# Performance work log

Hardware: AMD Instinct MI355X
Metric: run time of the kernel (lower is better)

The kernel has to match this reference:

```python
import jax, jax.numpy as jnp
import numpy as np

DIM = 256
D_STATE = 32
EXPAND = 2
E = EXPAND * DIM            # d_inner = 512
DT_RANK = (DIM + 15) // 16  # 16 (mamba default ceil(d_model/16))
D_CONV = 4                  # mamba default causal conv width
B = 4
L = 1024


def layernorm(x, g, b, eps=1e-5):
    m = jnp.mean(x, axis=-1, keepdims=True)
    v = jnp.var(x, axis=-1, keepdims=True)
    return (x - m) / jnp.sqrt(v + eps) * g + b


def dwconv(x_bcl, w, b, pad):
    # x_bcl: [B,C,L], w: [C,1,K] depthwise
    y = jax.lax.conv_general_dilated(
        x_bcl, w, window_strides=(1,), padding=[pad],
        feature_group_count=x_bcl.shape[1],
        dimension_numbers=('NCW', 'OIW', 'NCW'))
    return y + b[None, :, None]


def selective_scan(u, dt, A, Bm, Cm, D):
    # u,dt: [B,L,E]; A: [E,N]; Bm,Cm: [B,L,N]; D: [E]
    dA = jnp.exp(dt[..., None] * A)                                # [B,L,E,N]
    dBu = dt[..., None] * Bm[:, :, None, :] * u[..., None]         # [B,L,E,N]

    def step(h, inp):
        dA_t, dBu_t = inp
        h = dA_t * h + dBu_t
        return h, h

    h0 = jnp.zeros((u.shape[0], E, D_STATE), u.dtype)
    _, hs = jax.lax.scan(step, h0, (dA.transpose(1, 0, 2, 3), dBu.transpose(1, 0, 2, 3)))
    y = jnp.einsum('lben,bln->ble', hs, Cm)                        # [B,L,E]
    return y + u * D


def mamba(x, in_proj_w, ssm_conv_w, ssm_conv_b, x_proj_w,
          dt_proj_w, dt_proj_b, A_log, Dp, out_proj_w):
    xz = x @ in_proj_w.T                     # [B,L,2E]
    xin, z = xz[..., :E], xz[..., E:]
    # causal depthwise conv (pad left D_CONV-1) + SiLU
    xc = dwconv(xin.transpose(0, 2, 1), ssm_conv_w, ssm_conv_b, (D_CONV - 1, 0))
    u = jax.nn.silu(xc).transpose(0, 2, 1)   # [B,L,E]
    dbl = u @ x_proj_w.T                      # [B,L,dt_rank+2N]
    dt_r = dbl[..., :DT_RANK]
    Bm = dbl[..., DT_RANK:DT_RANK + D_STATE]
    Cm = dbl[..., DT_RANK + D_STATE:]
    dt = jax.nn.softplus(dt_r @ dt_proj_w.T + dt_proj_b)  # [B,L,E]
    A = -jnp.exp(A_log)                                    # [E,N]
    y = selective_scan(u, dt, A, Bm, Cm, Dp)
    y = y * jax.nn.silu(z)
    return y @ out_proj_w.T


def setup_inputs() -> dict:
    key = jax.random.key(0)
    ks = jax.random.split(key, 12)
    f = lambda k, s, sc=0.02: jax.random.normal(k, s, jnp.float32) * sc
    dt_init = jnp.exp(jax.random.uniform(ks[10], (E,), jnp.float32,
                                         np.log(1e-3), np.log(1e-1)))
    dt_bias = dt_init + jnp.log(-jnp.expm1(-dt_init))  # inverse softplus
    A_log = jnp.log(jnp.tile(jnp.arange(1, D_STATE + 1, dtype=jnp.float32), (E, 1)))
    return {
        'x': jax.random.normal(ks[0], (B, L, DIM), jnp.float32),
        'norm1_g': jnp.ones((DIM,), jnp.float32), 'norm1_b': jnp.zeros((DIM,), jnp.float32),
        'conv_w': f(ks[1], (DIM, 1, 3), 0.1), 'conv_b': jnp.zeros((DIM,), jnp.float32),
        'in_proj_w': f(ks[2], (2 * E, DIM)),
        'ssm_conv_w': f(ks[3], (E, 1, D_CONV), 0.1), 'ssm_conv_b': jnp.zeros((E,), jnp.float32),
        'x_proj_w': f(ks[4], (DT_RANK + 2 * D_STATE, E)),
        'dt_proj_w': f(ks[5], (E, DT_RANK), 0.1), 'dt_proj_b': dt_bias,
        'A_log': A_log, 'Dp': jnp.ones((E,), jnp.float32),
        'out_proj_w': f(ks[6], (DIM, E)),
        'norm2_g': jnp.ones((DIM,), jnp.float32), 'norm2_b': jnp.zeros((DIM,), jnp.float32),
        'mlp_w1': f(ks[7], (4 * DIM, DIM)), 'mlp_b1': jnp.zeros((4 * DIM,), jnp.float32),
        'mlp_w2': f(ks[8], (DIM, 4 * DIM)), 'mlp_b2': jnp.zeros((DIM,), jnp.float32),
    }


def reference(x, norm1_g, norm1_b, conv_w, conv_b, in_proj_w, ssm_conv_w,
              ssm_conv_b, x_proj_w, dt_proj_w, dt_proj_b, A_log, Dp,
              out_proj_w, norm2_g, norm2_b, mlp_w1, mlp_b1, mlp_w2, mlp_b2):
    res = x
    h = layernorm(x, norm1_g, norm1_b)
    # local depthwise conv, kernel 3, same padding
    h_conv = dwconv(h.transpose(0, 2, 1), conv_w, conv_b, (1, 1)).transpose(0, 2, 1)
    h = mamba(h_conv + h, in_proj_w, ssm_conv_w, ssm_conv_b, x_proj_w,
              dt_proj_w, dt_proj_b, A_log, Dp, out_proj_w)
    h = res + h  # drop_path = identity (eval)
    m = layernorm(h, norm2_g, norm2_b)
    m = jax.nn.gelu(m @ mlp_w1.T + mlp_b1, approximate=False) @ mlp_w2.T + mlp_b2
    return h + m
```

## Files before the change

### kernel.cpp

```cpp
#include <hip/hip_runtime.h>
#include <hip/hip_bf16.h>
#include <math.h>

#define BATCH 4
#define LSEQ  1024
#define DIM   256
#define ESZ   512
#define NST   32
#define RNK   16
#define MROWS 4096
#define NCH   64
#define CHL   16

typedef __attribute__((ext_vector_type(8))) short bf16x8;
typedef __attribute__((ext_vector_type(4))) float f32x4;

__device__ __forceinline__ float silu_f(float v) { return v / (1.f + __expf(-v)); }
__device__ __forceinline__ float softplus_f(float v) {
    return (v > 20.f) ? v : log1pf(__expf(v));
}
__device__ __forceinline__ float bs2f(short s) {
    union { unsigned int u; float f; } v;
    v.u = ((unsigned int)(unsigned short)s) << 16;
    return v.f;
}
__device__ __forceinline__ short f2bs(float f) {
    __hip_bfloat16 h = __float2bfloat16(f);
    return *(short*)&h;
}

template <int N> __device__ __forceinline__ void waitvm() {
    if constexpr (N == 0) asm volatile("s_waitcnt vmcnt(0)" ::: "memory");
    else if constexpr (N == 4) asm volatile("s_waitcnt vmcnt(4)" ::: "memory");
    else if constexpr (N == 6) asm volatile("s_waitcnt vmcnt(6)" ::: "memory");
    else if constexpr (N == 9) asm volatile("s_waitcnt vmcnt(9)" ::: "memory");
    else static_assert(N == 0, "add literal");
}
__device__ __forceinline__ void fence_sched() {
    __builtin_amdgcn_sched_barrier(0);
    asm volatile("" ::: "memory");
}

__global__ __launch_bounds__(256) void prep_kernel(
    const float* __restrict__ ipw, const float* __restrict__ opw,
    const float* __restrict__ w1,  const float* __restrict__ w2,
    const float* __restrict__ xpw, __hip_bfloat16* __restrict__ dst,
    const float* __restrict__ x, const float* __restrict__ g,
    const float* __restrict__ b, const float* __restrict__ cw,
    const float* __restrict__ cb, __hip_bfloat16* __restrict__ hm)
{
    if (blockIdx.x < 936) {
        int i = blockIdx.x * 256 + threadIdx.x;
        if (i >= 239616) return;
        const float* s; int off;
        if      (i < 65536)  { s = ipw; off = i; }
        else if (i < 98304)  { s = opw; off = i - 65536; }
        else if (i < 163840) { s = w1;  off = i - 98304; }
        else if (i < 229376) { s = w2;  off = i - 163840; }
        else                 { s = xpw; off = i - 229376; }
        float4 v = ((const float4*)s)[off];
        union { __hip_bfloat16 h[4]; short4 s4; } u;
        u.h[0] = __float2bfloat16(v.x);
        u.h[1] = __float2bfloat16(v.y);
        u.h[2] = __float2bfloat16(v.z);
        u.h[3] = __float2bfloat16(v.w);
        ((short4*)dst)[i] = u.s4;
        return;
    }
    const int row = blockIdx.x - 936;
    const int l   = row & (LSEQ - 1);
    const int d   = threadIdx.x;
    const float gc = g[d], bc = b[d];

    float xc = x[row * DIM + d];
    float xl = (l > 0)        ? x[(row - 1) * DIM + d] : 0.f;
    float xr = (l < LSEQ - 1) ? x[(row + 1) * DIM + d] : 0.f;

    float a[6] = { xc, xc * xc, xl, xl * xl, xr, xr * xr };
    #pragma unroll
    for (int o = 32; o > 0; o >>= 1)
        #pragma unroll
        for (int j = 0; j < 6; ++j) a[j] += __shfl_down(a[j], o, 64);
    __shared__ float red[4][6];
    if ((d & 63) == 0)
        #pragma unroll
        for (int j = 0; j < 6; ++j) red[d >> 6][j] = a[j];
    __syncthreads();
    float t[6];
    #pragma unroll
    for (int j = 0; j < 6; ++j)
        t[j] = red[0][j] + red[1][j] + red[2][j] + red[3][j];

    auto ln = [&](float v, float s, float s2) {
        float m  = s * (1.f / DIM);
        float vr = s2 * (1.f / DIM) - m * m;
        return (v - m) * rsqrtf(vr + 1e-5f) * gc + bc;
    };
    float ln_c = ln(xc, t[0], t[1]);
    float acc  = cw[d * 3 + 1] * ln_c + cb[d] + ln_c;
    if (l > 0)        acc += cw[d * 3 + 0] * ln(xl, t[2], t[3]);
    if (l < LSEQ - 1) acc += cw[d * 3 + 2] * ln(xr, t[4], t[5]);
    hm[row * DIM + d] = __float2bfloat16(acc);
}

#define EPI_NONE      0
#define EPI_GELU      2
#define EPI_RES       3
#define EPI_BIAS_RES  4

template <int BM, int BN, int EPI, int OUT_BF16>
__global__ __launch_bounds__(256) void gemm_lds(
    const __hip_bfloat16* __restrict__ A, int lda,
    const __hip_bfloat16* __restrict__ W, int ldw,
    void* __restrict__ Cout, int ldc, int K,
    const float* __restrict__ bias,
    const float* __restrict__ res, int ldres)
{
    constexpr int BK  = 64;
    constexpr int WTN = BN / 4;
    constexpr int BNF = WTN / 16;
    constexpr int AMF = BM / 16;
    constexpr int AIT = (BM * 8) / 256;
    constexpr int WIT = (BN * 8) / 256;
    constexpr int NLD = AIT + WIT;

    __shared__ __hip_bfloat16 As[2][BM * BK];
    __shared__ __hip_bfloat16 Ws[2][BN * BK];

    const int tid  = threadIdx.x;
    const int lane = tid & 63;
    const int wave = tid >> 6;
    const int wn   = wave * WTN;
    const int m0   = blockIdx.x * BM;
    const int n0   = blockIdx.y * BN;
    const int q    = lane >> 4;
    const int lr   = lane & 15;
    const int sx   = (lr & 7) << 4;

    const __hip_bfloat16* Ab = A + (long)m0 * lda;
    const __hip_bfloat16* Wb = W + (long)n0 * ldw;

    f32x4 acc[AMF][BNF];
    #pragma unroll
    for (int i = 0; i < AMF; ++i)
        #pragma unroll
        for (int j = 0; j < BNF; ++j)
            acc[i][j] = (f32x4){0.f, 0.f, 0.f, 0.f};

    auto stage = [&](int s, int k0) {
        #pragma unroll
        for (int it = 0; it < AIT; ++it) {
            const int g   = it * 256 + tid;
            const int row = g >> 3;
            const int scc = (g & 7) ^ (row & 7);
            __builtin_amdgcn_global_load_lds(
                (const __attribute__((address_space(1))) void*)
                    (Ab + (long)row * lda + k0 + scc * 8),
                (__attribute__((address_space(3))) void*)
                    (&As[s][(it * 256 + wave * 64) * 8]),
                16, 0, 0);
        }
        #pragma unroll
        for (int it = 0; it < WIT; ++it) {
            const int g   = it * 256 + tid;
            const int row = g >> 3;
            const int scc = (g & 7) ^ (row & 7);
            __builtin_amdgcn_global_load_lds(
                (const __attribute__((address_space(1))) void*)
                    (Wb + (long)row * ldw + k0 + scc * 8),
                (__attribute__((address_space(3))) void*)
                    (&Ws[s][(it * 256 + wave * 64) * 8]),
                16, 0, 0);
        }
    };

    stage(0, 0);
    if (BK < K) stage(1, BK);

    int cur = 0;
    for (int k0 = 0; k0 < K; k0 += BK) {
        if (k0 + BK < K) waitvm<NLD>(); else waitvm<0>();
        __builtin_amdgcn_s_barrier();
        fence_sched();
        #pragma unroll
        for (int ks = 0; ks < 2; ++ks) {
            const int co = (ks * 64 + q * 16) ^ sx;
            bf16x8 af[AMF], bfr[BNF];
            #pragma unroll
            for (int i = 0; i < AMF; ++i)
                af[i] = *(const bf16x8*)(
                    (const char*)&As[cur][0] + (i * 16 + lr) * 128 + co);
            #pragma unroll
            for (int j = 0; j < BNF; ++j)
                bfr[j] = *(const bf16x8*)(
                    (const char*)&Ws[cur][0] + (wn + j * 16 + lr) * 128 + co);
            #pragma unroll
            for (int i = 0; i < AMF; ++i)
                #pragma unroll
                for (int j = 0; j < BNF; ++j)
                    acc[i][j] = __builtin_amdgcn_mfma_f32_16x16x32_bf16(
                        af[i], bfr[j], acc[i][j], 0, 0, 0);
        }
        fence_sched();
        __builtin_amdgcn_s_barrier();
        fence_sched();
        if (k0 + 2 * BK < K) stage(cur, k0 + 2 * BK);
        cur ^= 1;
    }

    #pragma unroll
    for (int i = 0; i < AMF; ++i) {
        #pragma unroll
        for (int j = 0; j < BNF; ++j) {
            const int col  = n0 + wn + j * 16 + lr;
            const int rowb = m0 + i * 16 + q * 4;
            #pragma unroll
            for (int r = 0; r < 4; ++r) {
                const int row = rowb + r;
                float v = acc[i][j][r];
                if (EPI == EPI_GELU) {
                    v += bias[col];
                    v = 0.5f * v * (1.f + erff(v * 0.70710678118654752f));
                } else if (EPI == EPI_RES) {
                    v += res[(long)row * ldres + col];
                } else if (EPI == EPI_BIAS_RES) {
                    v += bias[col] + res[(long)row * ldres + col];
                }
                if (OUT_BF16)
                    ((__hip_bfloat16*)Cout)[(long)row * ldc + col] = __float2bfloat16(v);
                else
                    ((float*)Cout)[(long)row * ldc + col] = v;
            }
        }
    }
}

__global__ __launch_bounds__(256) void outproj_ln_kernel(
    const __hip_bfloat16* __restrict__ A,
    const __hip_bfloat16* __restrict__ W,
    const float* __restrict__ xres,
    const float* __restrict__ g, const float* __restrict__ b,
    float* __restrict__ hres,
    __hip_bfloat16* __restrict__ h1)
{
    constexpr int BM = 16, BN = 256, BK = 64, K = 512;
    constexpr int NLD = 9;
    __shared__ __hip_bfloat16 As[2][BM * BK];
    __shared__ __hip_bfloat16 Ws[2][BN * BK];
    __shared__ float lnt[BM][BN + 4];
    __shared__ float lnm[BM], lni[BM];

    const int tid  = threadIdx.x;
    const int lane = tid & 63;
    const int wave = tid >> 6;
    const int wn   = wave * 64;
    const int m0   = blockIdx.x * BM;
    const int q    = lane >> 4;
    const int lr   = lane & 15;
    const int sx   = (lr & 7) << 4;

    const __hip_bfloat16* Ab = A + (long)m0 * K;

    f32x4 acc[4];
    #pragma unroll
    for (int j = 0; j < 4; ++j) acc[j] = (f32x4){0.f, 0.f, 0.f, 0.f};

    auto stage = [&](int s, int k0) {
        {
            const int ch = wave * 32 + lane;
            if (lane < 32) {
                const int row = ch >> 3;
                const int scc = (ch & 7) ^ (row & 7);
                __builtin_amdgcn_global_load_lds(
                    (const __attribute__((address_space(1))) void*)
                        (Ab + (long)row * K + k0 + scc * 8),
                    (__attribute__((address_space(3))) void*)
                        (&As[s][(wave * 32) * 8]),
                    16, 0, 0);
            }
        }
        #pragma unroll
        for (int it = 0; it < 8; ++it) {
            const int gW  = it * 256 + tid;
            const int row = gW >> 3;
            const int scc = (gW & 7) ^ (row & 7);
            __builtin_amdgcn_global_load_lds(
                (const __attribute__((address_space(1))) void*)
                    (W + (long)row * K + k0 + scc * 8),
                (__attribute__((address_space(3))) void*)
                    (&Ws[s][(it * 256 + wave * 64) * 8]),
                16, 0, 0);
        }
    };

    stage(0, 0);
    stage(1, BK);

    int cur = 0;
    for (int k0 = 0; k0 < K; k0 += BK) {
        if (k0 + BK < K) waitvm<NLD>(); else waitvm<0>();
        __builtin_amdgcn_s_barrier();
        fence_sched();
        #pragma unroll
        for (int ks = 0; ks < 2; ++ks) {
            const int co = (ks * 64 + q * 16) ^ sx;
            bf16x8 af = *(const bf16x8*)((const char*)&As[cur][0] + lr * 128 + co);
            #pragma unroll
            for (int j = 0; j < 4; ++j) {
                bf16x8 bfr = *(const bf16x8*)(
                    (const char*)&Ws[cur][0] + (wn + j * 16 + lr) * 128 + co);
                acc[j] = __builtin_amdgcn_mfma_f32_16x16x32_bf16(af, bfr, acc[j], 0, 0, 0);
            }
        }
        fence_sched();
        __builtin_amdgcn_s_barrier();
        fence_sched();
        if (k0 + 2 * BK < K) stage(cur, k0 + 2 * BK);
        cur ^= 1;
    }

    #pragma unroll
    for (int j = 0; j < 4; ++j) {
        const int col = wn + j * 16 + lr;
        #pragma unroll
        for (int r = 0; r < 4; ++r) {
            const int row = q * 4 + r;
            float v = acc[j][r] + xres[(long)(m0 + row) * DIM + col];
            hres[(long)(m0 + row) * DIM + col] = v;
            lnt[row][col] = v;
        }
    }
    __syncthreads();

    {
        const int rr = tid >> 4, cc = tid & 15;
        float s = 0.f, s2 = 0.f;
        #pragma unroll
        for (int k = 0; k < 16; ++k) {
            float v = lnt[rr][cc + k * 16];
            s += v; s2 += v * v;
        }
        #pragma unroll
        for (int m = 8; m > 0; m >>= 1) {
            s  += __shfl_xor(s,  m, 64);
            s2 += __shfl_xor(s2, m, 64);
        }
        if (cc == 0) {
            float mean = s * (1.f / DIM);
            float var  = s2 * (1.f / DIM) - mean * mean;
            lnm[rr] = mean;
            lni[rr] = rsqrtf(var + 1e-5f);
        }
    }
    __syncthreads();

    #pragma unroll
    for (int j = 0; j < 4; ++j) {
        const int col = wn + j * 16 + lr;
        const float gc = g[col], bc = b[col];
        #pragma unroll
        for (int r = 0; r < 4; ++r) {
            const int row = q * 4 + r;
            float v = lnt[row][col];
            h1[(long)(m0 + row) * DIM + col] =
                __float2bfloat16((v - lnm[row]) * lni[row] * gc + bc);
        }
    }
}

__global__ __launch_bounds__(256) void xproj_conv_mfma(
    const __hip_bfloat16* __restrict__ xz,
    const float* __restrict__ scw, const float* __restrict__ scb,
    const __hip_bfloat16* __restrict__ W,
    float* __restrict__ C)
{
    constexpr int LS = 72;
    __shared__ __hip_bfloat16 As[64 * LS];
    __shared__ __hip_bfloat16 Ws[80 * LS];
    const int tid  = threadIdx.x;
    const int lane = tid & 63;
    const int wave = tid >> 6;
    const int wm   = wave * 16;
    const int m0   = blockIdx.x * 64;
    const int srow = tid >> 3;
    const int scol = (tid & 7) * 8;
    const int q    = lane >> 4;
    const int lr   = lane & 15;

    f32x4 acc[5];
    #pragma unroll
    for (int j = 0; j < 5; ++j) acc[j] = (f32x4){0.f, 0.f, 0.f, 0.f};

    auto mk_u2 = [&](int k0, bf16x8& u0, bf16x8& u1) {
        const int e0 = k0 + scol;
        float4 w4[8]; float cbv[8];
        #pragma unroll
        for (int j = 0; j < 8; ++j) {
            w4[j]  = *(const float4*)(scw + (e0 + j) * 4);
            cbv[j] = scb[e0 + j];
        }
        #pragma unroll
        for (int r = 0; r < 2; ++r) {
            const int bl = m0 + r * 32 + srow;
            const int l  = bl & (LSEQ - 1);
            const __hip_bfloat16* xp = xz + (long)bl * 1024 + e0;
            bf16x8 x3 = *(const bf16x8*)(xp);
            bf16x8 x0 = (l >= 3) ? *(const bf16x8*)(xp - 3 * 1024) : (bf16x8){0,0,0,0,0,0,0,0};
            bf16x8 x1 = (l >= 2) ? *(const bf16x8*)(xp - 2 * 1024) : (bf16x8){0,0,0,0,0,0,0,0};
            bf16x8 x2 = (l >= 1) ? *(const bf16x8*)(xp - 1 * 1024) : (bf16x8){0,0,0,0,0,0,0,0};
            bf16x8 o;
            #pragma unroll
            for (int j = 0; j < 8; ++j) {
                float a = cbv[j]
                    + w4[j].x * bs2f(x0[j]) + w4[j].y * bs2f(x1[j])
                    + w4[j].z * bs2f(x2[j]) + w4[j].w * bs2f(x3[j]);
                o[j] = f2bs(silu_f(a));
            }
            if (r == 0) u0 = o; else u1 = o;
        }
    };

    bf16x8 uc[2];
    float4 wr[3];
    mk_u2(0, uc[0], uc[1]);
    #pragma unroll
    for (int r = 0; r < 3; ++r) {
        int row = r * 32 + srow;
        wr[r] = (row < 80) ? *(const float4*)(W + (long)row * 512 + scol)
                           : make_float4(0.f, 0.f, 0.f, 0.f);
    }

    for (int k0 = 0; k0 < 512; k0 += 64) {
        __syncthreads();
        #pragma unroll
        for (int r = 0; r < 2; ++r)
            *(bf16x8*)(&As[(r * 32 + srow) * LS + scol]) = uc[r];
        #pragma unroll
        for (int r = 0; r < 3; ++r) {
            int row = r * 32 + srow;
            if (row < 80) *(float4*)(&Ws[row * LS + scol]) = wr[r];
        }
        __syncthreads();
        if (k0 + 64 < 512) {
            mk_u2(k0 + 64, uc[0], uc[1]);
            #pragma unroll
            for (int r = 0; r < 3; ++r) {
                int row = r * 32 + srow;
                if (row < 80)
                    wr[r] = *(const float4*)(W + (long)row * 512 + k0 + 64 + scol);
            }
        }
        #pragma unroll
        for (int ks = 0; ks < 2; ++ks) {
            bf16x8 af = *(const bf16x8*)(&As[(wm + lr) * LS + ks * 32 + q * 8]);
            #pragma unroll
            for (int j = 0; j < 5; ++j) {
                bf16x8 bf = *(const bf16x8*)(&Ws[(j * 16 + lr) * LS + ks * 32 + q * 8]);
                acc[j] = __builtin_amdgcn_mfma_f32_16x16x32_bf16(af, bf, acc[j], 0, 0, 0);
            }
        }
    }
    #pragma unroll
    for (int j = 0; j < 5; ++j)
        #pragma unroll
        for (int r = 0; r < 4; ++r)
            C[(long)(m0 + wm + q * 4 + r) * 80 + j * 16 + lr] = acc[j][r];
}

__global__ __launch_bounds__(256) void scan_s1(
    const __hip_bfloat16* __restrict__ xz, const float* __restrict__ dbl,
    const float* __restrict__ dtw, const float* __restrict__ dtb,
    const float* __restrict__ A_log,
    const float* __restrict__ scw, const float* __restrict__ scb,
    __hip_bfloat16* __restrict__ P, __hip_bfloat16* __restrict__ Q)
{
    const int tid = threadIdx.x;
    const int e  = ((blockIdx.x & 1) << 8) + tid;
    const int bc = blockIdx.x >> 1;
    const int c  = bc & (NCH - 1);
    const int b  = bc >> 6;

    __shared__ float sD[CHL][80];
    for (int g = tid; g < CHL * 20; g += 256) {
        int r = g / 20, cg = (g % 20) * 4;
        *(float4*)&sD[r][cg] =
            *(const float4*)(dbl + ((long)b * LSEQ + c * CHL + r) * 80 + cg);
    }

    float Aen[NST];
    #pragma unroll
    for (int qd = 0; qd < 8; ++qd) {
        float4 a4 = *(const float4*)(A_log + e * NST + qd * 4);
        Aen[qd * 4 + 0] = -__expf(a4.x);
        Aen[qd * 4 + 1] = -__expf(a4.y);
        Aen[qd * 4 + 2] = -__expf(a4.z);
        Aen[qd * 4 + 3] = -__expf(a4.w);
    }
    float cw4[4];
    #pragma unroll
    for (int k = 0; k < 4; ++k) cw4[k] = scw[e * 4 + k];
    const float cbe = scb[e];

    float4 wq[4];
    #pragma unroll
    for (int qd = 0; qd < 4; ++qd)
        wq[qd] = *(const float4*)(dtw + e * RNK + qd * 4);
    const float dtbe = dtb[e];

    const int l0 = c * CHL;
    const long rowbase = ((long)b * LSEQ) * 1024 + e;
    float xw0, xw1, xw2;
    if (c == 0) { xw0 = xw1 = xw2 = 0.f; }
    else {
        xw0 = __bfloat162float(xz[rowbase + (long)(l0 - 3) * 1024]);
        xw1 = __bfloat162float(xz[rowbase + (long)(l0 - 2) * 1024]);
        xw2 = __bfloat162float(xz[rowbase + (long)(l0 - 1) * 1024]);
    }

    float Pv[NST], Qv[NST];
    #pragma unroll
    for (int n = 0; n < NST; ++n) { Pv[n] = 1.f; Qv[n] = 0.f; }
    __syncthreads();

    for (int t = 0; t < CHL; ++t) {
        const int l = l0 + t;
        float xw3 = __bfloat162float(xz[rowbase + (long)l * 1024]);
        float u = silu_f(cbe + cw4[0]*xw0 + cw4[1]*xw1 + cw4[2]*xw2 + cw4[3]*xw3);
        xw0 = xw1; xw1 = xw2; xw2 = xw3;

        float4 d0 = *(const float4*)&sD[t][0];
        float4 d1 = *(const float4*)&sD[t][4];
        float4 d2 = *(const float4*)&sD[t][8];
        float4 d3 = *(const float4*)&sD[t][12];
        float raw = dtbe
            + wq[0].x*d0.x + wq[0].y*d0.y + wq[0].z*d0.z + wq[0].w*d0.w
            + wq[1].x*d1.x + wq[1].y*d1.y + wq[1].z*d1.z + wq[1].w*d1.w
            + wq[2].x*d2.x + wq[2].y*d2.y + wq[2].z*d2.z + wq[2].w*d2.w
            + wq[3].x*d3.x + wq[3].y*d3.y + wq[3].z*d3.z + wq[3].w*d3.w;
        float dt = softplus_f(raw);
        float xx = dt * u;

        #pragma unroll
        for (int qd = 0; qd < 8; ++qd) {
            float4 b4 = *(const float4*)&sD[t][16 + qd * 4];
            #pragma unroll
            for (int j = 0; j < 4; ++j) {
                const int n = qd * 4 + j;
                float bn = (j == 0) ? b4.x : (j == 1) ? b4.y : (j == 2) ? b4.z : b4.w;
                float dA = __expf(dt * Aen[n]);
                Pv[n] *= dA;
                Qv[n] = fmaf(dA, Qv[n], xx * bn);
            }
        }
    }
    const long pb = ((long)(b * NCH + c) * NST) * ESZ + e;
    #pragma unroll
    for (int n = 0; n < NST; ++n) {
        P[pb + (long)n * ESZ] = __float2bfloat16(Pv[n]);
        Q[pb + (long)n * ESZ] = __float2bfloat16(Qv[n]);
    }
}

__global__ __launch_bounds__(256) void scan_s2(
    __hip_bfloat16* __restrict__ P, const __hip_bfloat16* __restrict__ Q)
{
    const int tg = blockIdx.x * 256 + threadIdx.x;
    const int e  = tg & (ESZ - 1);
    const int n  = (tg >> 9) & (NST - 1);
    const int b  = tg >> 14;
    float h = 0.f;
    #pragma unroll 16
    for (int c = 0; c < NCH; ++c) {
        const long idx = ((long)(b * NCH + c) * NST + n) * ESZ + e;
        float Pv = __bfloat162float(P[idx]);
        float Qv = __bfloat162float(Q[idx]);
        P[idx] = __float2bfloat16(h);
        h = fmaf(Pv, h, Qv);
    }
}

__global__ __launch_bounds__(256) void scan_s3(
    const __hip_bfloat16* __restrict__ xz, const float* __restrict__ dbl,
    const float* __restrict__ dtw, const float* __restrict__ dtb,
    const float* __restrict__ A_log,
    const float* __restrict__ scw, const float* __restrict__ scb,
    const float* __restrict__ Dp, const __hip_bfloat16* __restrict__ H,
    __hip_bfloat16* __restrict__ yg)
{
    const int tid = threadIdx.x;
    const int e  = ((blockIdx.x & 1) << 8) + tid;
    const int bc = blockIdx.x >> 1;
    const int c  = bc & (NCH - 1);
    const int b  = bc >> 6;

    __shared__ float sD[CHL][80];
    for (int g = tid; g < CHL * 20; g += 256) {
        int r = g / 20, cg = (g % 20) * 4;
        *(float4*)&sD[r][cg] =
            *(const float4*)(dbl + ((long)b * LSEQ + c * CHL + r) * 80 + cg);
    }

    float Aen[NST];
    #pragma unroll
    for (int qd = 0; qd < 8; ++qd) {
        float4 a4 = *(const float4*)(A_log + e * NST + qd * 4);
        Aen[qd * 4 + 0] = -__expf(a4.x);
        Aen[qd * 4 + 1] = -__expf(a4.y);
        Aen[qd * 4 + 2] = -__expf(a4.z);
        Aen[qd * 4 + 3] = -__expf(a4.w);
    }
    float cw4[4];
    #pragma unroll
    for (int k = 0; k < 4; ++k) cw4[k] = scw[e * 4 + k];
    const float cbe = scb[e];
    const float dpe = Dp[e];

    float4 wq[4];
    #pragma unroll
    for (int qd = 0; qd < 4; ++qd)
        wq[qd] = *(const float4*)(dtw + e * RNK + qd * 4);
    const float dtbe = dtb[e];

    float h[NST];
    const long pb = ((long)(b * NCH + c) * NST) * ESZ + e;
    #pragma unroll
    for (int n = 0; n < NST; ++n)
        h[n] = __bfloat162float(H[pb + (long)n * ESZ]);

    const int l0 = c * CHL;
    const long rowbase = ((long)b * LSEQ) * 1024 + e;
    float xw0, xw1, xw2;
    if (c == 0) { xw0 = xw1 = xw2 = 0.f; }
    else {
        xw0 = __bfloat162float(xz[rowbase + (long)(l0 - 3) * 1024]);
        xw1 = __bfloat162float(xz[rowbase + (long)(l0 - 2) * 1024]);
        xw2 = __bfloat162float(xz[rowbase + (long)(l0 - 1) * 1024]);
    }
    __syncthreads();

    for (int t = 0; t < CHL; ++t) {
        const int l = l0 + t;
        const long bl = (long)b * LSEQ + l;
        float xw3 = __bfloat162float(xz[rowbase + (long)l * 1024]);
        float u = silu_f(cbe + cw4[0]*xw0 + cw4[1]*xw1 + cw4[2]*xw2 + cw4[3]*xw3);
        xw0 = xw1; xw1 = xw2; xw2 = xw3;

        float4 d0 = *(const float4*)&sD[t][0];
        float4 d1 = *(const float4*)&sD[t][4];
        float4 d2 = *(const float4*)&sD[t][8];
        float4 d3 = *(const float4*)&sD[t][12];
        float raw = dtbe
            + wq[0].x*d0.x + wq[0].y*d0.y + wq[0].z*d0.z + wq[0].w*d0.w
            + wq[1].x*d1.x + wq[1].y*d1.y + wq[1].z*d1.z + wq[1].w*d1.w
            + wq[2].x*d2.x + wq[2].y*d2.y + wq[2].z*d2.z + wq[2].w*d2.w
            + wq[3].x*d3.x + wq[3].y*d3.y + wq[3].z*d3.z + wq[3].w*d3.w;
        float dt = softplus_f(raw);
        float xx = dt * u;

        float y = 0.f;
        #pragma unroll
        for (int qd = 0; qd < 8; ++qd) {
            float4 b4 = *(const float4*)&sD[t][16 + qd * 4];
            float4 c4 = *(const float4*)&sD[t][48 + qd * 4];
            #pragma unroll
            for (int j = 0; j < 4; ++j) {
                const int n = qd * 4 + j;
                float bn = (j == 0) ? b4.x : (j == 1) ? b4.y : (j == 2) ? b4.z : b4.w;
                float cn = (j == 0) ? c4.x : (j == 1) ? c4.y : (j == 2) ? c4.z : c4.w;
                float dA = __expf(dt * Aen[n]);
                h[n] = fmaf(dA, h[n], xx * bn);
                y = fmaf(h[n], cn, y);
            }
        }
        y += u * dpe;
        float z = __bfloat162float(xz[rowbase + (long)l * 1024 + ESZ]);
        yg[bl * ESZ + e] = __float2bfloat16(y * silu_f(z));
    }
}

extern "C" void kernel_launch(void* const* d_in, const int* in_sizes, int n_in,
                              void* d_out, int out_size, void* d_ws, size_t ws_size,
                              hipStream_t stream)
{
    const float* x    = (const float*)d_in[0];
    const float* n1g  = (const float*)d_in[1];
    const float* n1b  = (const float*)d_in[2];
    const float* cw   = (const float*)d_in[3];
    const float* cb   = (const float*)d_in[4];
    const float* ipw  = (const float*)d_in[5];
    const float* scw  = (const float*)d_in[6];
    const float* scb  = (const float*)d_in[7];
    const float* xpw  = (const float*)d_in[8];
    const float* dtw  = (const float*)d_in[9];
    const float* dtbi = (const float*)d_in[10];
    const float* alog = (const float*)d_in[11];
    const float* dp   = (const float*)d_in[12];
    const float* opw  = (const float*)d_in[13];
    const float* n2g  = (const float*)d_in[14];
    const float* n2b  = (const float*)d_in[15];
    const float* w1   = (const float*)d_in[16];
    const float* b1   = (const float*)d_in[17];
    const float* w2   = (const float*)d_in[18];
    const float* b2   = (const float*)d_in[19];
    float* out = (float*)d_out;

    float* ws = (float*)d_ws;
    __hip_bfloat16* hmb  = (__hip_bfloat16*)(ws + 0);
    __hip_bfloat16* xzb  = (__hip_bfloat16*)(ws + 524288);
    float*          dbl  = ws + 3670016;
    __hip_bfloat16* P    = (__hip_bfloat16*)(ws + 5046272);
    __hip_bfloat16* Q    = (__hip_bfloat16*)(ws + 7143424);
    __hip_bfloat16* ygb  = (__hip_bfloat16*)(ws + 9240576);
    float*          hres = ws + 10289152;
    __hip_bfloat16* h1b  = (__hip_bfloat16*)(ws + 11337728);
    __hip_bfloat16* midb = (__hip_bfloat16*)(ws + 11862016);
    __hip_bfloat16* wb   = (__hip_bfloat16*)(ws + 13959168);
    __hip_bfloat16* ipwb = wb;
    __hip_bfloat16* opwb = wb + 262144;
    __hip_bfloat16* w1b  = wb + 393216;
    __hip_bfloat16* w2b  = wb + 655360;
    __hip_bfloat16* xpwb = wb + 917504;

    prep_kernel<<<5032, 256, 0, stream>>>(ipw, opw, w1, w2, xpw, wb,
                                          x, n1g, n1b, cw, cb, hmb);
    gemm_lds<64, 128, EPI_NONE, 1><<<dim3(64, 8), 256, 0, stream>>>(
        hmb, 256, ipwb, 256, xzb, 1024, 256, nullptr, nullptr, 0);
    xproj_conv_mfma<<<64, 256, 0, stream>>>(xzb, scw, scb, xpwb, dbl);
    scan_s1<<<512, 256, 0, stream>>>(xzb, dbl, dtw, dtbi, alog, scw, scb, P, Q);
    scan_s2<<<256, 256, 0, stream>>>(P, Q);
    scan_s3<<<512, 256, 0, stream>>>(xzb, dbl, dtw, dtbi, alog, scw, scb, dp, P, ygb);
    outproj_ln_kernel<<<256, 256, 0, stream>>>(ygb, opwb, x, n2g, n2b, hres, h1b);
    gemm_lds<64, 128, EPI_GELU, 1><<<dim3(64, 8), 256, 0, stream>>>(
        h1b, 256, w1b, 256, midb, 1024, 256, b1, nullptr, 0);
    gemm_lds<64, 64, EPI_BIAS_RES, 0><<<dim3(64, 4), 256, 0, stream>>>(
        midb, 1024, w2b, 1024, out, 256, 1024, b2, hres, 256);
}
```

Baseline: 231.7 us.

## Fuse scan stage 3 with out-projection GEMM and LayerNorm in one kernel

Merges the final chunked-scan stage with the out_proj GEMM, residual add and second LayerNorm. Each 512-thread block computes a 16-token chunk's gated y for all 512 channels into swizzled LDS, then runs the MFMA GEMM against double-buffered out_proj weights and the LN epilogue. This removes the global round trip of the bf16 y tensor and one kernel launch. In exchange it halves the grid to 256 blocks, raises LDS use (weights, Ys and LN tile), and leaves the scan part with fewer resident waves.

```diff
diff --git a/kernel.cpp b/kernel.cpp
--- a/kernel.cpp
+++ b/kernel.cpp
@@ -235,139 +235,6 @@
     }
 }
 
-__global__ __launch_bounds__(256) void outproj_ln_kernel(
-    const __hip_bfloat16* __restrict__ A,
-    const __hip_bfloat16* __restrict__ W,
-    const float* __restrict__ xres,
-    const float* __restrict__ g, const float* __restrict__ b,
-    float* __restrict__ hres,
-    __hip_bfloat16* __restrict__ h1)
-{
-    constexpr int BM = 16, BN = 256, BK = 64, K = 512;
-    constexpr int NLD = 9;
-    __shared__ __hip_bfloat16 As[2][BM * BK];
-    __shared__ __hip_bfloat16 Ws[2][BN * BK];
-    __shared__ float lnt[BM][BN + 4];
-    __shared__ float lnm[BM], lni[BM];
-
-    const int tid  = threadIdx.x;
-    const int lane = tid & 63;
-    const int wave = tid >> 6;
-    const int wn   = wave * 64;
-    const int m0   = blockIdx.x * BM;
-    const int q    = lane >> 4;
-    const int lr   = lane & 15;
-    const int sx   = (lr & 7) << 4;
-
-    const __hip_bfloat16* Ab = A + (long)m0 * K;
-
-    f32x4 acc[4];
-    #pragma unroll
-    for (int j = 0; j < 4; ++j) acc[j] = (f32x4){0.f, 0.f, 0.f, 0.f};
-
-    auto stage = [&](int s, int k0) {
-        {
-            const int ch = wave * 32 + lane;
-            if (lane < 32) {
-                const int row = ch >> 3;
-                const int scc = (ch & 7) ^ (row & 7);
-                __builtin_amdgcn_global_load_lds(
-                    (const __attribute__((address_space(1))) void*)
-                        (Ab + (long)row * K + k0 + scc * 8),
-                    (__attribute__((address_space(3))) void*)
-                        (&As[s][(wave * 32) * 8]),
-                    16, 0, 0);
-            }
-        }
-        #pragma unroll
-        for (int it = 0; it < 8; ++it) {
-            const int gW  = it * 256 + tid;
-            const int row = gW >> 3;
-            const int scc = (gW & 7) ^ (row & 7);
-            __builtin_amdgcn_global_load_lds(
-                (const __attribute__((address_space(1))) void*)
-                    (W + (long)row * K + k0 + scc * 8),
-                (__attribute__((address_space(3))) void*)
-                    (&Ws[s][(it * 256 + wave * 64) * 8]),
-                16, 0, 0);
-        }
-    };
-
-    stage(0, 0);
-    stage(1, BK);
-
-    int cur = 0;
-    for (int k0 = 0; k0 < K; k0 += BK) {
-        if (k0 + BK < K) waitvm<NLD>(); else waitvm<0>();
-        __builtin_amdgcn_s_barrier();
-        fence_sched();
-        #pragma unroll
-        for (int ks = 0; ks < 2; ++ks) {
-            const int co = (ks * 64 + q * 16) ^ sx;
-            bf16x8 af = *(const bf16x8*)((const char*)&As[cur][0] + lr * 128 + co);
-            #pragma unroll
-            for (int j = 0; j < 4; ++j) {
-                bf16x8 bfr = *(const bf16x8*)(
-                    (const char*)&Ws[cur][0] + (wn + j * 16 + lr) * 128 + co);
-                acc[j] = __builtin_amdgcn_mfma_f32_16x16x32_bf16(af, bfr, acc[j], 0, 0, 0);
-            }
-        }
-        fence_sched();
-        __builtin_amdgcn_s_barrier();
-        fence_sched();
-        if (k0 + 2 * BK < K) stage(cur, k0 + 2 * BK);
-        cur ^= 1;
-    }
-
-    #pragma unroll
-    for (int j = 0; j < 4; ++j) {
-        const int col = wn + j * 16 + lr;
-        #pragma unroll
-        for (int r = 0; r < 4; ++r) {
-            const int row = q * 4 + r;
-            float v = acc[j][r] + xres[(long)(m0 + row) * DIM + col];
-            hres[(long)(m0 + row) * DIM + col] = v;
-            lnt[row][col] = v;
-        }
-    }
-    __syncthreads();
-
-    {
-        const int rr = tid >> 4, cc = tid & 15;
-        float s = 0.f, s2 = 0.f;
-        #pragma unroll
-        for (int k = 0; k < 16; ++k) {
-            float v = lnt[rr][cc + k * 16];
-            s += v; s2 += v * v;
-        }
-        #pragma unroll
-        for (int m = 8; m > 0; m >>= 1) {
-            s  += __shfl_xor(s,  m, 64);
-            s2 += __shfl_xor(s2, m, 64);
-        }
-        if (cc == 0) {
-            float mean = s * (1.f / DIM);
-            float var  = s2 * (1.f / DIM) - mean * mean;
-            lnm[rr] = mean;
-            lni[rr] = rsqrtf(var + 1e-5f);
-        }
-    }
-    __syncthreads();
-
-    #pragma unroll
-    for (int j = 0; j < 4; ++j) {
-        const int col = wn + j * 16 + lr;
-        const float gc = g[col], bc = b[col];
-        #pragma unroll
-        for (int r = 0; r < 4; ++r) {
-            const int row = q * 4 + r;
-            float v = lnt[row][col];
-            h1[(long)(m0 + row) * DIM + col] =
-                __float2bfloat16((v - lnm[row]) * lni[row] * gc + bc);
-        }
-    }
-}
-
 __global__ __launch_bounds__(256) void xproj_conv_mfma(
     const __hip_bfloat16* __restrict__ xz,
     const float* __restrict__ scw, const float* __restrict__ scb,
@@ -579,26 +446,57 @@
     }
 }
 
-__global__ __launch_bounds__(256) void scan_s3(
+__global__ __launch_bounds__(512) void scan3_outproj_ln(
     const __hip_bfloat16* __restrict__ xz, const float* __restrict__ dbl,
     const float* __restrict__ dtw, const float* __restrict__ dtb,
     const float* __restrict__ A_log,
     const float* __restrict__ scw, const float* __restrict__ scb,
     const float* __restrict__ Dp, const __hip_bfloat16* __restrict__ H,
-    __hip_bfloat16* __restrict__ yg)
+    const __hip_bfloat16* __restrict__ W,
+    const float* __restrict__ xres,
+    const float* __restrict__ g, const float* __restrict__ b_,
+    float* __restrict__ hres,
+    __hip_bfloat16* __restrict__ h1)
 {
-    const int tid = threadIdx.x;
-    const int e  = ((blockIdx.x & 1) << 8) + tid;
-    const int bc = blockIdx.x >> 1;
-    const int c  = bc & (NCH - 1);
-    const int b  = bc >> 6;
-
+    constexpr int BK = 64, K = 512;
+    constexpr int NLD = 4;
     __shared__ float sD[CHL][80];
-    for (int g = tid; g < CHL * 20; g += 256) {
-        int r = g / 20, cg = (g % 20) * 4;
+    __shared__ __hip_bfloat16 Ys[CHL * ESZ];
+    __shared__ __hip_bfloat16 Wsh[2][256 * BK];
+    __shared__ float lnt[CHL][DIM + 4];
+    __shared__ float lnm[CHL], lni[CHL];
+
+    const int tid  = threadIdx.x;
+    const int lane = tid & 63;
+    const int wave = tid >> 6;
+    const int q    = lane >> 4;
+    const int lr   = lane & 15;
+    const int e    = tid;
+    const int bc   = blockIdx.x;
+    const int c    = bc & (NCH - 1);
+    const int b    = bc >> 6;
+    const int m0   = bc * CHL;
+
+    if (tid < CHL * 20) {
+        int r = tid / 20, cg = (tid % 20) * 4;
         *(float4*)&sD[r][cg] =
             *(const float4*)(dbl + ((long)b * LSEQ + c * CHL + r) * 80 + cg);
     }
+
+    auto stageW = [&](int s, int k0) {
+        #pragma unroll
+        for (int it = 0; it < 4; ++it) {
+            const int gW  = it * 512 + tid;
+            const int row = gW >> 3;
+            const int scc = (gW & 7) ^ (row & 7);
+            __builtin_amdgcn_global_load_lds(
+                (const __attribute__((address_space(1))) void*)
+                    (W + (long)row * K + k0 + scc * 8),
+                (__attribute__((address_space(3))) void*)
+                    (&Wsh[s][(it * 512 + wave * 64) * 8]),
+                16, 0, 0);
+        }
+    };
 
     float Aen[NST];
     #pragma unroll
@@ -638,9 +536,13 @@
     }
     __syncthreads();
 
+    stageW(0, 0);
+    stageW(1, BK);
+    fence_sched();
+
+    char* yb = (char*)Ys;
     for (int t = 0; t < CHL; ++t) {
         const int l = l0 + t;
-        const long bl = (long)b * LSEQ + l;
         float xw3 = __bfloat162float(xz[rowbase + (long)l * 1024]);
         float u = silu_f(cbe + cw4[0]*xw0 + cw4[1]*xw1 + cw4[2]*xw2 + cw4[3]*xw3);
         xw0 = xw1; xw1 = xw2; xw2 = xw3;
@@ -674,7 +576,87 @@
         }
         y += u * dpe;
         float z = __bfloat162float(xz[rowbase + (long)l * 1024 + ESZ]);
-        yg[bl * ESZ + e] = __float2bfloat16(y * silu_f(z));
+        *(short*)(yb + t * 1024 + ((e << 1) ^ ((t & 7) << 4))) =
+            f2bs(y * silu_f(z));
+    }
+    __syncthreads();
+
+    const int wn = wave * 32;
+    const int sx = (lr & 7) << 4;
+    f32x4 acc[2];
+    acc[0] = (f32x4){0.f, 0.f, 0.f, 0.f};
+    acc[1] = (f32x4){0.f, 0.f, 0.f, 0.f};
+
+    int cur = 0;
+    for (int k0 = 0; k0 < K; k0 += BK) {
+        if (k0 + BK < K) waitvm<NLD>(); else waitvm<0>();
+        __builtin_amdgcn_s_barrier();
+        fence_sched();
+        #pragma unroll
+        for (int ks = 0; ks < 2; ++ks) {
+            const int colb = (k0 + ks * 32 + q * 8) << 1;
+            bf16x8 af = *(const bf16x8*)(yb + lr * 1024 + (colb ^ ((lr & 7) << 4)));
+            const int co = (ks * 64 + q * 16) ^ sx;
+            #pragma unroll
+            for (int j = 0; j < 2; ++j) {
+                bf16x8 bfr = *(const bf16x8*)(
+                    (const char*)&Wsh[cur][0] + (wn + j * 16 + lr) * 128 + co);
+                acc[j] = __builtin_amdgcn_mfma_f32_16x16x32_bf16(af, bfr, acc[j], 0, 0, 0);
+            }
+        }
+        fence_sched();
+        __builtin_amdgcn_s_barrier();
+        fence_sched();
+        if (k0 + 2 * BK < K) stageW(cur, k0 + 2 * BK);
+        cur ^= 1;
+    }
+
+    #pragma unroll
+    for (int j = 0; j < 2; ++j) {
+        const int col = wn + j * 16 + lr;
+        #pragma unroll
+        for (int r = 0; r < 4; ++r) {
+            const int row = q * 4 + r;
+            float v = acc[j][r] + xres[(long)(m0 + row) * DIM + col];
+            hres[(long)(m0 + row) * DIM + col] = v;
+            lnt[row][col] = v;
+        }
+    }
+    __syncthreads();
+
+    {
+        const int rr = tid >> 5, cc = tid & 31;
+        float s = 0.f, s2 = 0.f;
+        #pragma unroll
+        for (int k = 0; k < 8; ++k) {
+            float v = lnt[rr][cc + k * 32];
+            s += v; s2 += v * v;
+        }
+        #pragma unroll
+        for (int m = 16; m > 0; m >>= 1) {
+            s  += __shfl_xor(s,  m, 64);
+            s2 += __shfl_xor(s2, m, 64);
+        }
+        if (cc == 0) {
+            float mean = s * (1.f / DIM);
+            float var  = s2 * (1.f / DIM) - mean * mean;
+            lnm[rr] = mean;
+            lni[rr] = rsqrtf(var + 1e-5f);
+        }
+    }
+    __syncthreads();
+
+    #pragma unroll
+    for (int j = 0; j < 2; ++j) {
+        const int col = wn + j * 16 + lr;
+        const float gc = g[col], bc = b_[col];
+        #pragma unroll
+        for (int r = 0; r < 4; ++r) {
+            const int row = q * 4 + r;
+            float v = lnt[row][col];
+            h1[(long)(m0 + row) * DIM + col] =
+                __float2bfloat16((v - lnm[row]) * lni[row] * gc + bc);
+        }
     }
 }
 
@@ -710,7 +692,6 @@
     float*          dbl  = ws + 3670016;
     __hip_bfloat16* P    = (__hip_bfloat16*)(ws + 5046272);
     __hip_bfloat16* Q    = (__hip_bfloat16*)(ws + 7143424);
-    __hip_bfloat16* ygb  = (__hip_bfloat16*)(ws + 9240576);
     float*          hres = ws + 10289152;
     __hip_bfloat16* h1b  = (__hip_bfloat16*)(ws + 11337728);
     __hip_bfloat16* midb = (__hip_bfloat16*)(ws + 11862016);
@@ -728,8 +709,9 @@
     xproj_conv_mfma<<<64, 256, 0, stream>>>(xzb, scw, scb, xpwb, dbl);
     scan_s1<<<512, 256, 0, stream>>>(xzb, dbl, dtw, dtbi, alog, scw, scb, P, Q);
     scan_s2<<<256, 256, 0, stream>>>(P, Q);
-    scan_s3<<<512, 256, 0, stream>>>(xzb, dbl, dtw, dtbi, alog, scw, scb, dp, P, ygb);
-    outproj_ln_kernel<<<256, 256, 0, stream>>>(ygb, opwb, x, n2g, n2b, hres, h1b);
+    scan3_outproj_ln<<<256, 512, 0, stream>>>(
+        xzb, dbl, dtw, dtbi, alog, scw, scb, dp, P, opwb,
+        x, n2g, n2b, hres, h1b);
     gemm_lds<64, 128, EPI_GELU, 1><<<dim3(64, 8), 256, 0, stream>>>(
         h1b, 256, w1b, 256, midb, 1024, 256, b1, nullptr, 0);
     gemm_lds<64, 64, EPI_BIAS_RES, 0><<<dim3(64, 4), 256, 0, stream>>>(
```

After: 223.4 us. -3.6%, faster.
